# Kernel tuning notes

Measured on AMD Instinct MI355X. Metric: run time of the kernel, lower is better.

## Reference

```python
import jax, jax.numpy as jnp
import numpy as np

D = 1024      # input_dim == memory_dim
HID = 1024    # hid_dim
NEG = 1e30


def setup_inputs() -> dict:
    key = jax.random.key(0)
    ks = jax.random.split(key, 9)
    N, LD, LM = 8, 2048, 512
    s = 1.0 / np.sqrt(D)
    return {
        "input": jax.random.normal(ks[0], (N, LD, D), jnp.float32),
        "memory": jax.random.normal(ks[1], (N, LM, D), jnp.float32),
        "mask": jnp.ones((N, LM), jnp.float32),
        # input_linear_1 / memory_linear_1: Linear(d, 1, bias=False)
        "in1_w": jax.random.normal(ks[2], (D,), jnp.float32) * s,
        "mem1_w": jax.random.normal(ks[3], (D,), jnp.float32) * s,
        # input_linear_2 / memory_linear_2: Linear(d, hid, bias=True), stored [d, hid]
        "in2_w": jax.random.normal(ks[4], (D, HID), jnp.float32) * s,
        "in2_b": jax.random.normal(ks[5], (HID,), jnp.float32) * s,
        "mem2_w": jax.random.normal(ks[6], (D, HID), jnp.float32) * s,
        "mem2_b": jax.random.normal(ks[7], (HID,), jnp.float32) * s,
    }


def reference(input, memory, mask, in1_w, mem1_w, in2_w, in2_b, mem2_w, mem2_b):
    # dropout=0.0 / eval mode -> identity
    dot_scale = jnp.asarray(np.sqrt(D), input.dtype)
    input_dot = jnp.einsum("nld,d->nl", input, in1_w)[:, :, None]      # [N,Ld,1]
    memory_dot = jnp.einsum("nmd,d->nm", memory, mem1_w)[:, None, :]   # [N,1,Lm]
    cross_dot = jnp.einsum("nld,nmd->nlm", input, memory) / dot_scale  # [N,Ld,Lm]
    att = input_dot + memory_dot + cross_dot
    att = att - NEG * (1.0 - mask[:, None, :])

    inp2 = jnp.einsum("nld,dh->nlh", input, in2_w) + in2_b    # [N,Ld,hid]
    mem2 = jnp.einsum("nmd,dh->nmh", memory, mem2_w) + mem2_b  # [N,Lm,hid]

    weight_one = jax.nn.softmax(att, axis=-1)                 # [N,Ld,Lm]
    output_one = jnp.einsum("nlm,nmh->nlh", weight_one, mem2)  # [N,Ld,hid]

    weight_two = jax.nn.softmax(jnp.max(att, axis=-1), axis=-1)  # [N,Ld]
    output_two = jnp.einsum("nl,nlh->nh", weight_two, inp2)[:, None, :]  # [N,1,hid]

    out = jnp.concatenate(
        [inp2, output_one, inp2 * output_one, output_two * output_one], axis=-1
    )  # [N,Ld,4*hid]
    return out, mem2
```

## Files before the change

### kernel.cpp

```cpp
#include <hip/hip_runtime.h>

typedef unsigned short u16;
typedef __attribute__((ext_vector_type(8))) short short8;
typedef __attribute__((ext_vector_type(4))) float f32x4;
typedef __attribute__((ext_vector_type(4))) unsigned short u16x4;

#define NSEQ 8
#define LD 2048
#define LM 512
#define DD 1024
#define HID 1024
#define M1 (NSEQ*LD)
#define M2 (NSEQ*LM)

#define GLOAD_LDS16(gp, lp) __builtin_amdgcn_global_load_lds( \
    (const __attribute__((address_space(1))) unsigned int*)(gp), \
    (__attribute__((address_space(3))) unsigned int*)(lp), 16, 0, 0)

__device__ __forceinline__ u16 f2bf(float f) {
    union { float f; unsigned int i; } v; v.f = f;
    unsigned int r = v.i + 0x7fffu + ((v.i >> 16) & 1u);
    return (u16)(r >> 16);
}
__device__ __forceinline__ float bf2f(u16 u) {
    union { unsigned int i; float f; } v; v.i = ((unsigned int)u) << 16; return v.f;
}

__global__ __launch_bounds__(256) void prep_rows2(
    const float* __restrict__ input, const float* __restrict__ memory,
    const float* __restrict__ in1_w, const float* __restrict__ mem1_w,
    const float* __restrict__ mask,
    u16* __restrict__ input_bf16, u16* __restrict__ memory_bf16,
    float* __restrict__ idot, float* __restrict__ mdotm) {
    const int row = blockIdx.x, t = threadIdx.x;
    const float* src; const float* w; u16* dst;
    if (row < M1) { src = input + (size_t)row * DD; w = in1_w;
                    dst = input_bf16 + (size_t)row * DD; }
    else { const int rm = row - M1; src = memory + (size_t)rm * DD; w = mem1_w;
           dst = memory_bf16 + (size_t)rm * DD; }
    f32x4 v = *(const f32x4*)(src + t * 4);
    f32x4 wv = *(const f32x4*)(w + t * 4);
    u16x4 o;
    #pragma unroll
    for (int i = 0; i < 4; i++) o[i] = f2bf(v[i]);
    *(u16x4*)(dst + t * 4) = o;
    float s = v[0]*wv[0] + v[1]*wv[1] + v[2]*wv[2] + v[3]*wv[3];
    #pragma unroll
    for (int off = 32; off; off >>= 1) s += __shfl_down(s, off);
    __shared__ float red[4];
    if ((t & 63) == 0) red[t >> 6] = s;
    __syncthreads();
    if (t == 0) {
        const float d = red[0] + red[1] + red[2] + red[3];
        if (row < M1) idot[row] = d;
        else { const int rm = row - M1;
               mdotm[rm] = d - 1e30f * (1.0f - mask[rm]); }
    }
}

__global__ void wtrans(const float* __restrict__ s0, const float* __restrict__ s1,
                       u16* __restrict__ d0, u16* __restrict__ d1) {
    __shared__ float tile[32][33];
    const float* src = blockIdx.z ? s1 : s0;
    u16* dst = blockIdx.z ? d1 : d0;
    const int c0 = blockIdx.x * 32, r0 = blockIdx.y * 32;
    const int tx = threadIdx.x, ty = threadIdx.y;
    #pragma unroll
    for (int yy = ty; yy < 32; yy += 8)
        tile[yy][tx] = src[(size_t)(r0 + yy) * DD + c0 + tx];
    __syncthreads();
    #pragma unroll
    for (int yy = ty; yy < 32; yy += 8)
        dst[(size_t)(c0 + yy) * DD + r0 + tx] = f2bf(tile[tx][yy]);
}

__global__ void transpose_f32_to_bf16(const float* __restrict__ src,
                                      u16* __restrict__ dst,
                                      int R, int C, size_t sn, size_t dn) {
    __shared__ float tile[32][33];
    src += (size_t)blockIdx.z * sn;
    dst += (size_t)blockIdx.z * dn;
    const int c0 = blockIdx.x * 32, r0 = blockIdx.y * 32;
    const int tx = threadIdx.x, ty = threadIdx.y;
    #pragma unroll
    for (int yy = ty; yy < 32; yy += 8)
        tile[yy][tx] = src[(size_t)(r0 + yy) * C + c0 + tx];
    __syncthreads();
    #pragma unroll
    for (int yy = ty; yy < 32; yy += 8)
        dst[(size_t)(c0 + yy) * R + r0 + tx] = f2bf(tile[tx][yy]);
}

template <int NT>
__global__ __launch_bounds__(512, 1) void gemm256(
    const u16* __restrict__ A, const u16* __restrict__ B,
    int lda, int ldb,
    float* __restrict__ out0, int ldc, const float* __restrict__ bias) {
    constexpr int BUFE = (256 + 128) * 64;
    __shared__ __align__(16) u16 lds[3 * BUFE];
    const int t = threadIdx.x;
    const int lane = t & 63, wave = t >> 6;
    const int wm = wave >> 2, wn = wave & 3;
    const int lr = lane & 15, kg = lane >> 4;
    const int bid = blockIdx.y * 8 + blockIdx.x;
    const int swz = (bid & 7) * gridDim.y + (bid >> 3);
    const int m0 = (swz >> 3) * 256, n0 = (swz & 7) * 128;

    const int srow = lane >> 3;
    const u16* gA[4];
    const u16* gB[2];
    #pragma unroll
    for (int i = 0; i < 4; i++) {
        const int c = wave * 4 + i;
        const int colb = ((lane & 7) * 16) ^ ((((c << 2) + (lane >> 4)) & 7) << 4);
        gA[i] = A + (size_t)(m0 + c * 8 + srow) * lda + (colb >> 1);
    }
    #pragma unroll
    for (int i = 0; i < 2; i++) {
        const int c = wave * 2 + i;
        const int colb = ((lane & 7) * 16) ^ ((((c << 2) + (lane >> 4)) & 7) << 4);
        gB[i] = B + (size_t)(n0 + c * 8 + srow) * ldb + (colb >> 1);
    }
    int offA[8], offB[2];
    #pragma unroll
    for (int i = 0; i < 8; i++) {
        const int row = wm * 128 + i * 16 + lr;
        offA[i] = (row * 128 + kg * 16) ^ (((row >> 1) & 7) << 4);
    }
    #pragma unroll
    for (int j = 0; j < 2; j++) {
        const int row = wn * 32 + j * 16 + lr;
        offB[j] = (256 * 64 * 2 + row * 128 + kg * 16) ^ (((row >> 1) & 7) << 4);
    }

    f32x4 acc[8][2];
    #pragma unroll
    for (int i = 0; i < 8; i++)
        #pragma unroll
        for (int j = 0; j < 2; j++) acc[i][j] = (f32x4){0.f, 0.f, 0.f, 0.f};

    #define STAGE(tt, buf) do {                                             \
        u16* la_ = &lds[(buf) * BUFE];                                      \
        u16* lb_ = la_ + 256 * 64;                                          \
        const int ko_ = (tt) * 64;                                          \
        _Pragma("unroll")                                                   \
        for (int i_ = 0; i_ < 4; i_++)                                      \
            GLOAD_LDS16(gA[i_] + ko_, la_ + (wave * 4 + i_) * 512);         \
        _Pragma("unroll")                                                   \
        for (int i_ = 0; i_ < 2; i_++)                                      \
            GLOAD_LDS16(gB[i_] + ko_, lb_ + (wave * 2 + i_) * 512);         \
    } while (0)

    STAGE(0, 0);
    STAGE(1, 1);
    asm volatile("s_waitcnt vmcnt(6)" ::: "memory");
    __builtin_amdgcn_s_barrier();
    __builtin_amdgcn_sched_barrier(0);

    int cb = 0, sb = 2;
    for (int tt = 0; tt < NT; ++tt) {
        if (tt + 2 < NT) STAGE(tt + 2, sb);
        __builtin_amdgcn_sched_barrier(0);
        const char* bb = (const char*)&lds[cb * BUFE];
        short8 bfr[2][2];
        #pragma unroll
        for (int j = 0; j < 2; j++)
            #pragma unroll
            for (int kh = 0; kh < 2; kh++)
                bfr[j][kh] = *(const short8*)(bb + (offB[j] ^ (kh * 64)));
        #pragma unroll
        for (int p = 0; p < 4; p++) {
            short8 af[2][2];
            #pragma unroll
            for (int q = 0; q < 2; q++)
                #pragma unroll
                for (int kh = 0; kh < 2; kh++)
                    af[q][kh] = *(const short8*)(bb + (offA[2 * p + q] ^ (kh * 64)));
            __builtin_amdgcn_s_setprio(1);
            #pragma unroll
            for (int q = 0; q < 2; q++)
                #pragma unroll
                for (int j = 0; j < 2; j++)
                    #pragma unroll
                    for (int kh = 0; kh < 2; kh++)
                        acc[2 * p + q][j] = __builtin_amdgcn_mfma_f32_16x16x32_bf16(
                            af[q][kh], bfr[j][kh], acc[2 * p + q][j], 0, 0, 0);
            __builtin_amdgcn_s_setprio(0);
        }
        if (tt + 2 < NT)      asm volatile("s_waitcnt vmcnt(6)" ::: "memory");
        else if (tt + 1 < NT) asm volatile("s_waitcnt vmcnt(0)" ::: "memory");
        __builtin_amdgcn_s_barrier();
        __builtin_amdgcn_sched_barrier(0);
        cb = (cb == 2) ? 0 : cb + 1;
        sb = (sb == 2) ? 0 : sb + 1;
    }
    #undef STAGE

    #pragma unroll
    for (int i = 0; i < 8; i++) {
        #pragma unroll
        for (int j = 0; j < 2; j++) {
            const int col = n0 + wn * 32 + j * 16 + lr;
            #pragma unroll
            for (int r = 0; r < 4; r++) {
                const int row = m0 + wm * 128 + i * 16 + kg * 4 + r;
                out0[(size_t)row * ldc + col] = acc[i][j][r] + bias[col];
            }
        }
    }
}

__global__ __launch_bounds__(512, 2) void fused_gemm(
    const u16* __restrict__ A1, const u16* __restrict__ B1,
    const u16* __restrict__ A2, const u16* __restrict__ B2,
    float* __restrict__ out0,
    const float* __restrict__ bias, const float* __restrict__ ot) {
    constexpr int BUFE = (256 + 128) * 64;
    __shared__ __align__(16) u16 lds[3 * BUFE];
    const int t = threadIdx.x;
    const int lane = t & 63, wave = t >> 6;
    const int wm = wave >> 2, wn = wave & 3;
    const int lr = lane & 15, kg = lane >> 4;
    const int bid = blockIdx.y * 8 + blockIdx.x;
    const int swz = (bid & 7) * gridDim.y + (bid >> 3);
    const int m0 = (swz >> 3) * 256, n0 = (swz & 7) * 128;
    const int nb = m0 / LD;
    const u16* B2p = B2 + (size_t)nb * HID * LM;

    const int srow = lane >> 3;
    int colbA[4], colbB[2];
    const u16* gA[4];
    const u16* gB[2];
    #pragma unroll
    for (int i = 0; i < 4; i++) {
        const int c = wave * 4 + i;
        colbA[i] = ((lane & 7) * 16) ^ ((((c << 2) + (lane >> 4)) & 7) << 4);
        gA[i] = A1 + (size_t)(m0 + c * 8 + srow) * DD + (colbA[i] >> 1);
    }
    #pragma unroll
    for (int i = 0; i < 2; i++) {
        const int c = wave * 2 + i;
        colbB[i] = ((lane & 7) * 16) ^ ((((c << 2) + (lane >> 4)) & 7) << 4);
        gB[i] = B1 + (size_t)(n0 + c * 8 + srow) * DD + (colbB[i] >> 1);
    }
    int offA[8], offB[2];
    #pragma unroll
    for (int i = 0; i < 8; i++) {
        const int row = wm * 128 + i * 16 + lr;
        offA[i] = (row * 128 + kg * 16) ^ (((row >> 1) & 7) << 4);
    }
    #pragma unroll
    for (int j = 0; j < 2; j++) {
        const int row = wn * 32 + j * 16 + lr;
        offB[j] = (256 * 64 * 2 + row * 128 + kg * 16) ^ (((row >> 1) & 7) << 4);
    }

    #define STAGE(tt, buf) do {                                             \
        u16* la_ = &lds[(buf) * BUFE];                                      \
        u16* lb_ = la_ + 256 * 64;                                          \
        const int ko_ = (tt) * 64;                                          \
        _Pragma("unroll")                                                   \
        for (int i_ = 0; i_ < 4; i_++)                                      \
            GLOAD_LDS16(gA[i_] + ko_, la_ + (wave * 4 + i_) * 512);         \
        _Pragma("unroll")                                                   \
        for (int i_ = 0; i_ < 2; i_++)                                      \
            GLOAD_LDS16(gB[i_] + ko_, lb_ + (wave * 2 + i_) * 512);         \
    } while (0)

    #define KLOOP(NT, ACC)                                                  \
    do {                                                                    \
        STAGE(0, 0);                                                        \
        STAGE(1, 1);                                                        \
        asm volatile("s_waitcnt vmcnt(6)" ::: "memory");                    \
        __builtin_amdgcn_s_barrier();                                       \
        __builtin_amdgcn_sched_barrier(0);                                  \
        int cb = 0, sb = 2;                                                 \
        for (int tt = 0; tt < (NT); ++tt) {                                 \
            if (tt + 2 < (NT)) STAGE(tt + 2, sb);                           \
            __builtin_amdgcn_sched_barrier(0);                              \
            const char* bb = (const char*)&lds[cb * BUFE];                  \
            short8 bfr[2][2];                                               \
            _Pragma("unroll")                                               \
            for (int j = 0; j < 2; j++)                                     \
                _Pragma("unroll")                                           \
                for (int kh = 0; kh < 2; kh++)                              \
                    bfr[j][kh] = *(const short8*)(bb + (offB[j] ^ (kh * 64))); \
            _Pragma("unroll")                                               \
            for (int p = 0; p < 4; p++) {                                   \
                short8 af[2][2];                                            \
                _Pragma("unroll")                                           \
                for (int q = 0; q < 2; q++)                                 \
                    _Pragma("unroll")                                       \
                    for (int kh = 0; kh < 2; kh++)                          \
                        af[q][kh] = *(const short8*)(bb + (offA[2 * p + q] ^ (kh * 64))); \
                __builtin_amdgcn_s_setprio(1);                              \
                _Pragma("unroll")                                           \
                for (int q = 0; q < 2; q++)                                 \
                    _Pragma("unroll")                                       \
                    for (int j = 0; j < 2; j++)                             \
                        _Pragma("unroll")                                   \
                        for (int kh = 0; kh < 2; kh++)                      \
                            ACC[2 * p + q][j] = __builtin_amdgcn_mfma_f32_16x16x32_bf16( \
                                af[q][kh], bfr[j][kh], ACC[2 * p + q][j], 0, 0, 0); \
                __builtin_amdgcn_s_setprio(0);                              \
            }                                                               \
            if (tt + 2 < (NT))      asm volatile("s_waitcnt vmcnt(6)" ::: "memory"); \
            else if (tt + 1 < (NT)) asm volatile("s_waitcnt vmcnt(0)" ::: "memory"); \
            __builtin_amdgcn_s_barrier();                                   \
            __builtin_amdgcn_sched_barrier(0);                              \
            cb = (cb == 2) ? 0 : cb + 1;                                    \
            sb = (sb == 2) ? 0 : sb + 1;                                    \
        }                                                                   \
    } while (0)

    f32x4 acc1[8][2], acc2[8][2];
    #pragma unroll
    for (int i = 0; i < 8; i++)
        #pragma unroll
        for (int j = 0; j < 2; j++) {
            acc1[i][j] = (f32x4){0.f, 0.f, 0.f, 0.f};
            acc2[i][j] = (f32x4){0.f, 0.f, 0.f, 0.f};
        }

    KLOOP(16, acc1);

    #pragma unroll
    for (int i = 0; i < 4; i++) {
        const int c = wave * 4 + i;
        gA[i] = A2 + (size_t)(m0 + c * 8 + srow) * LM + (colbA[i] >> 1);
    }
    #pragma unroll
    for (int i = 0; i < 2; i++) {
        const int c = wave * 2 + i;
        gB[i] = B2p + (size_t)(n0 + c * 8 + srow) * LM + (colbB[i] >> 1);
    }

    KLOOP(8, acc2);

    #undef KLOOP
    #undef STAGE

    #pragma unroll
    for (int i = 0; i < 8; i++) {
        #pragma unroll
        for (int j = 0; j < 2; j++) {
            const int col = n0 + wn * 32 + j * 16 + lr;
            const float b = bias[col];
            const float otv = ot[nb * HID + col];
            #pragma unroll
            for (int r = 0; r < 4; r++) {
                const int row = m0 + wm * 128 + i * 16 + kg * 4 + r;
                const size_t o = (size_t)row * 4096 + col;
                const float i2 = acc1[i][j][r] + b;
                const float o1 = acc2[i][j][r];
                out0[o] = i2;
                out0[o + 1024] = o1;
                out0[o + 2048] = i2 * o1;
                out0[o + 3072] = otv * o1;
            }
        }
    }
}

__global__ __launch_bounds__(512, 1) void att_softmax(
    const u16* __restrict__ A, const u16* __restrict__ B,
    const float* __restrict__ idot, const float* __restrict__ mdotm,
    u16* __restrict__ P, float* __restrict__ rowmax) {
    constexpr int ABUF = 64 * 64;
    constexpr int BBUF = 512 * 64;
    constexpr int BUFE = ABUF + BBUF;
    __shared__ __align__(16) u16 lds[2 * BUFE];
    const int t = threadIdx.x, lane = t & 63, wave = t >> 6;
    const int wm = wave >> 2, wn = wave & 3;
    const int lr = lane & 15, kg = lane >> 4;
    const int bid = blockIdx.x;
    const int swz = (bid & 7) * 32 + (bid >> 3);
    const int m0 = swz * 64;
    const int nb = m0 >> 11;
    const u16* Bp = B + (size_t)nb * LM * DD;

    const int srow = lane >> 3;
    const u16* gA;
    {
        const int c = wave;
        const int colb = ((lane & 7) * 16) ^ ((((c << 2) + (lane >> 4)) & 7) << 4);
        gA = A + (size_t)(m0 + c * 8 + srow) * DD + (colb >> 1);
    }
    const u16* gB[8];
    #pragma unroll
    for (int i = 0; i < 8; i++) {
        const int c = wave * 8 + i;
        const int colb = ((lane & 7) * 16) ^ ((((c << 2) + (lane >> 4)) & 7) << 4);
        gB[i] = Bp + (size_t)(c * 8 + srow) * DD + (colb >> 1);
    }
    int offA[2], offB[8];
    #pragma unroll
    for (int i = 0; i < 2; i++) {
        const int row = wm * 32 + i * 16 + lr;
        offA[i] = (row * 128 + kg * 16) ^ (((row >> 1) & 7) << 4);
    }
    #pragma unroll
    for (int j = 0; j < 8; j++) {
        const int row = wn * 128 + j * 16 + lr;
        offB[j] = (ABUF * 2 + row * 128 + kg * 16) ^ (((row >> 1) & 7) << 4);
    }

    f32x4 acc[2][8];
    #pragma unroll
    for (int i = 0; i < 2; i++)
        #pragma unroll
        for (int j = 0; j < 8; j++) acc[i][j] = (f32x4){0.f, 0.f, 0.f, 0.f};

    #define ASTAGE(tt, buf) do {                                            \
        u16* la_ = &lds[(buf) * BUFE];                                      \
        const int ko_ = (tt) * 64;                                          \
        GLOAD_LDS16(gA + ko_, la_ + wave * 512);                            \
        u16* lb_ = la_ + ABUF;                                              \
        _Pragma("unroll")                                                   \
        for (int i_ = 0; i_ < 8; i_++)                                      \
            GLOAD_LDS16(gB[i_] + ko_, lb_ + (wave * 8 + i_) * 512);         \
    } while (0)

    ASTAGE(0, 0);
    asm volatile("s_waitcnt vmcnt(0)" ::: "memory");
    __builtin_amdgcn_s_barrier();
    __builtin_amdgcn_sched_barrier(0);

    for (int tt = 0; tt < 16; ++tt) {
        if (tt + 1 < 16) ASTAGE(tt + 1, (tt + 1) & 1);
        __builtin_amdgcn_sched_barrier(0);
        const char* bb = (const char*)&lds[(tt & 1) * BUFE];
        short8 af[2][2];
        #pragma unroll
        for (int i = 0; i < 2; i++)
            #pragma unroll
            for (int kh = 0; kh < 2; kh++)
                af[i][kh] = *(const short8*)(bb + (offA[i] ^ (kh * 64)));
        #pragma unroll
        for (int j = 0; j < 8; j++) {
            short8 bf[2];
            #pragma unroll
            for (int kh = 0; kh < 2; kh++)
                bf[kh] = *(const short8*)(bb + (offB[j] ^ (kh * 64)));
            __builtin_amdgcn_s_setprio(1);
            #pragma unroll
            for (int i = 0; i < 2; i++)
                #pragma unroll
                for (int kh = 0; kh < 2; kh++)
                    acc[i][j] = __builtin_amdgcn_mfma_f32_16x16x32_bf16(
                        af[i][kh], bf[kh], acc[i][j], 0, 0, 0);
            __builtin_amdgcn_s_setprio(0);
        }
        if (tt + 1 < 16) asm volatile("s_waitcnt vmcnt(0)" ::: "memory");
        __builtin_amdgcn_s_barrier();
        __builtin_amdgcn_sched_barrier(0);
    }
    #undef ASTAGE

    float* redm = (float*)lds;
    float* reds = redm + 256;
    float mdv[8];
    #pragma unroll
    for (int j = 0; j < 8; j++)
        mdv[j] = mdotm[nb * LM + wn * 128 + j * 16 + lr];
    float idv[8];
    #pragma unroll
    for (int i = 0; i < 2; i++)
        #pragma unroll
        for (int r = 0; r < 4; r++)
            idv[i * 4 + r] = idot[m0 + wm * 32 + i * 16 + kg * 4 + r];
    float pm[8];
    #pragma unroll
    for (int i = 0; i < 2; i++)
        #pragma unroll
        for (int r = 0; r < 4; r++) {
            float mx = -3.0e38f;
            #pragma unroll
            for (int j = 0; j < 8; j++) {
                const float v = acc[i][j][r] * 0.03125f + idv[i * 4 + r] + mdv[j];
                acc[i][j][r] = v;
                mx = fmaxf(mx, v);
            }
            pm[i * 4 + r] = mx;
        }
    #pragma unroll
    for (int w = 1; w < 16; w <<= 1)
        #pragma unroll
        for (int q = 0; q < 8; q++) pm[q] = fmaxf(pm[q], __shfl_xor(pm[q], w));
    if (lr == 0) {
        #pragma unroll
        for (int i = 0; i < 2; i++)
            #pragma unroll
            for (int r = 0; r < 4; r++)
                redm[(wm * 32 + i * 16 + kg * 4 + r) * 4 + wn] = pm[i * 4 + r];
    }
    __syncthreads();
    float Mr[8], ps[8];
    #pragma unroll
    for (int i = 0; i < 2; i++)
        #pragma unroll
        for (int r = 0; r < 4; r++) {
            const int row = wm * 32 + i * 16 + kg * 4 + r;
            const float a = fmaxf(redm[row * 4 + 0], redm[row * 4 + 1]);
            const float b = fmaxf(redm[row * 4 + 2], redm[row * 4 + 3]);
            Mr[i * 4 + r] = fmaxf(a, b);
            float s = 0.f;
            #pragma unroll
            for (int j = 0; j < 8; j++) {
                const float e = __expf(acc[i][j][r] - Mr[i * 4 + r]);
                acc[i][j][r] = e;
                s += e;
            }
            ps[i * 4 + r] = s;
        }
    #pragma unroll
    for (int w = 1; w < 16; w <<= 1)
        #pragma unroll
        for (int q = 0; q < 8; q++) ps[q] += __shfl_xor(ps[q], w);
    if (lr == 0) {
        #pragma unroll
        for (int i = 0; i < 2; i++)
            #pragma unroll
            for (int r = 0; r < 4; r++)
                reds[(wm * 32 + i * 16 + kg * 4 + r) * 4 + wn] = ps[i * 4 + r];
    }
    __syncthreads();
    #pragma unroll
    for (int i = 0; i < 2; i++)
        #pragma unroll
        for (int r = 0; r < 4; r++) {
            const int row = wm * 32 + i * 16 + kg * 4 + r;
            const float inv = 1.0f / (reds[row * 4 + 0] + reds[row * 4 + 1] +
                                      reds[row * 4 + 2] + reds[row * 4 + 3]);
            if (wn == 0 && lr == 0) rowmax[m0 + row] = Mr[i * 4 + r];
            #pragma unroll
            for (int j = 0; j < 8; j++)
                P[(size_t)(m0 + row) * LM + wn * 128 + j * 16 + lr] =
                    f2bf(acc[i][j][r] * inv);
        }
}

__global__ __launch_bounds__(256) void xbar_partial(
    const float* __restrict__ rowmax, const u16* __restrict__ X,
    float* __restrict__ part) {
    const int lz = blockIdx.x, n = blockIdx.y, t = threadIdx.x;
    const float* rm = rowmax + (size_t)n * LD;
    float v[8];
    float m = -3.0e38f;
    #pragma unroll
    for (int i = 0; i < 8; i++) { v[i] = rm[t + i * 256]; m = fmaxf(m, v[i]); }
    #pragma unroll
    for (int off = 32; off; off >>= 1) m = fmaxf(m, __shfl_down(m, off));
    __shared__ float sm[4], ss[4];
    __shared__ float wl[256];
    if ((t & 63) == 0) sm[t >> 6] = m;
    __syncthreads();
    const float M = fmaxf(fmaxf(sm[0], sm[1]), fmaxf(sm[2], sm[3]));
    float s = 0.f;
    #pragma unroll
    for (int i = 0; i < 8; i++) s += __expf(v[i] - M);
    #pragma unroll
    for (int off = 32; off; off >>= 1) s += __shfl_down(s, off);
    if ((t & 63) == 0) ss[t >> 6] = s;
    __syncthreads();
    const float invS = 1.0f / (ss[0] + ss[1] + ss[2] + ss[3]);
    wl[t] = __expf(rm[lz * 256 + t] - M) * invS;
    __syncthreads();
    const u16* xp = X + ((size_t)n * LD + lz * 256) * DD + t * 4;
    f32x4 acc = {0.f, 0.f, 0.f, 0.f};
    #pragma unroll 4
    for (int l = 0; l < 256; l++) {
        u16x4 x = *(const u16x4*)(xp + (size_t)l * DD);
        const float w = wl[l];
        acc[0] += w * bf2f(x[0]); acc[1] += w * bf2f(x[1]);
        acc[2] += w * bf2f(x[2]); acc[3] += w * bf2f(x[3]);
    }
    *(f32x4*)&part[((size_t)n * 8 + lz) * HID + t * 4] = acc;
}

__global__ __launch_bounds__(256) void ot_final2(
    const float* __restrict__ part, const u16* __restrict__ Wt,
    const float* __restrict__ bias, float* __restrict__ ot) {
    const int hc = blockIdx.x, n = blockIdx.y, t = threadIdx.x;
    __shared__ float xb[HID];
    f32x4 s = {0.f, 0.f, 0.f, 0.f};
    #pragma unroll
    for (int i = 0; i < 8; i++) {
        f32x4 p = *(const f32x4*)&part[((size_t)n * 8 + i) * HID + t * 4];
        s[0] += p[0]; s[1] += p[1]; s[2] += p[2]; s[3] += p[3];
    }
    *(f32x4*)&xb[t * 4] = s;
    __syncthreads();
    const int h = hc * 128 + (t >> 1);
    const int d0 = (t & 1) * 512;
    float a = 0.f;
    #pragma unroll 4
    for (int d = 0; d < 512; d += 8) {
        short8 w8 = *(const short8*)&Wt[(size_t)h * DD + d0 + d];
        #pragma unroll
        for (int j = 0; j < 8; j++) a += bf2f((u16)w8[j]) * xb[d0 + d + j];
    }
    a += __shfl_xor(a, 1);
    if ((t & 1) == 0) ot[(size_t)n * HID + h] = a + bias[h];
}

extern "C" void kernel_launch(void* const* d_in, const int* in_sizes, int n_in,
                              void* d_out, int out_size, void* d_ws, size_t ws_size,
                              hipStream_t stream) {
    const float* input  = (const float*)d_in[0];
    const float* memory = (const float*)d_in[1];
    const float* mask   = (const float*)d_in[2];
    const float* in1_w  = (const float*)d_in[3];
    const float* mem1_w = (const float*)d_in[4];
    const float* in2_w  = (const float*)d_in[5];
    const float* in2_b  = (const float*)d_in[6];
    const float* mem2_w = (const float*)d_in[7];
    const float* mem2_b = (const float*)d_in[8];

    float* out = (float*)d_out;
    float* outTail = out + (size_t)M1 * 4096;

    char* ws = (char*)d_ws;
    size_t off = 0;
    auto alloc = [&](size_t bytes) -> void* {
        void* p = ws + off;
        off = (off + bytes + 255) & ~(size_t)255;
        return p;
    };
    u16* input_bf16  = (u16*)alloc((size_t)M1 * DD * 2);
    u16* memory_bf16 = (u16*)alloc((size_t)M2 * DD * 2);
    u16* in2_wt      = (u16*)alloc((size_t)HID * DD * 2);
    u16* mem2_wt     = (u16*)alloc((size_t)HID * DD * 2);
    u16* mem2t       = (u16*)alloc((size_t)NSEQ * HID * LM * 2);
    u16* P           = (u16*)alloc((size_t)M1 * LM * 2);
    float* idot      = (float*)alloc((size_t)M1 * 4);
    float* mdotm     = (float*)alloc((size_t)M2 * 4);
    float* rowmax    = (float*)alloc((size_t)M1 * 4);
    float* ot        = (float*)alloc((size_t)NSEQ * HID * 4);
    float* part      = (float*)alloc((size_t)NSEQ * 8 * HID * 4);

    prep_rows2<<<M1 + M2, 256, 0, stream>>>(input, memory, in1_w, mem1_w, mask,
                                            input_bf16, memory_bf16, idot, mdotm);
    wtrans<<<dim3(32, 32, 2), dim3(32, 8), 0, stream>>>(in2_w, mem2_w, in2_wt, mem2_wt);
    gemm256<16><<<dim3(8, M2 / 256), 512, 0, stream>>>(
        memory_bf16, mem2_wt, DD, DD, outTail, HID, mem2_b);
    transpose_f32_to_bf16<<<dim3(HID / 32, LM / 32, NSEQ), dim3(32, 8), 0, stream>>>(
        outTail, mem2t, LM, HID, (size_t)LM * HID, (size_t)HID * LM);
    att_softmax<<<M1 / 64, 512, 0, stream>>>(
        input_bf16, memory_bf16, idot, mdotm, P, rowmax);
    xbar_partial<<<dim3(8, NSEQ), 256, 0, stream>>>(rowmax, input_bf16, part);
    ot_final2<<<dim3(8, NSEQ), 256, 0, stream>>>(part, in2_wt, in2_b, ot);
    fused_gemm<<<dim3(8, M1 / 256), 512, 0, stream>>>(
        input_bf16, in2_wt, P, mem2t, out, in2_b, ot);
}
```

Baseline: 218.7 us.

## Shrink mem2 GEMM tile, triple-buffer att_softmax in halves, widen xbar split

Templates the mem2 projection GEMM on its A-tile height and launches it with 128-row tiles, doubling the block count so more CUs are busy on the small M2 problem. Restructures att_softmax to process the 512 memory columns in two 256-column passes with a three-stage LDS pipeline instead of double buffering. This cuts LDS per stage and overlaps loads better, at the cost of reloading the A tile twice. Splits xbar_partial across 32 chunks per sequence instead of 8 for more parallelism, which makes ot_final2 sum more partials.

Result: faster. 203.4 us (-7.0%).

```diff
diff --git a/kernel.cpp b/kernel.cpp
--- a/kernel.cpp
+++ b/kernel.cpp
@@ -91,12 +91,13 @@
         dst[(size_t)(c0 + yy) * R + r0 + tx] = f2bf(tile[tx][yy]);
 }
 
-template <int NT>
-__global__ __launch_bounds__(512, 1) void gemm256(
+template <int NT, int AI>
+__global__ __launch_bounds__(512, 1) void gemmT(
     const u16* __restrict__ A, const u16* __restrict__ B,
     int lda, int ldb,
     float* __restrict__ out0, int ldc, const float* __restrict__ bias) {
-    constexpr int BUFE = (256 + 128) * 64;
+    constexpr int BM = AI * 64;
+    constexpr int BUFE = (BM + 128) * 64;
     __shared__ __align__(16) u16 lds[3 * BUFE];
     const int t = threadIdx.x;
     const int lane = t & 63, wave = t >> 6;
@@ -104,14 +105,14 @@
     const int lr = lane & 15, kg = lane >> 4;
     const int bid = blockIdx.y * 8 + blockIdx.x;
     const int swz = (bid & 7) * gridDim.y + (bid >> 3);
-    const int m0 = (swz >> 3) * 256, n0 = (swz & 7) * 128;
+    const int m0 = (swz >> 3) * BM, n0 = (swz & 7) * 128;
 
     const int srow = lane >> 3;
-    const u16* gA[4];
+    const u16* gA[AI];
     const u16* gB[2];
     #pragma unroll
-    for (int i = 0; i < 4; i++) {
-        const int c = wave * 4 + i;
+    for (int i = 0; i < AI; i++) {
+        const int c = wave * AI + i;
         const int colb = ((lane & 7) * 16) ^ ((((c << 2) + (lane >> 4)) & 7) << 4);
         gA[i] = A + (size_t)(m0 + c * 8 + srow) * lda + (colb >> 1);
     }
@@ -121,39 +122,43 @@
         const int colb = ((lane & 7) * 16) ^ ((((c << 2) + (lane >> 4)) & 7) << 4);
         gB[i] = B + (size_t)(n0 + c * 8 + srow) * ldb + (colb >> 1);
     }
-    int offA[8], offB[2];
-    #pragma unroll
-    for (int i = 0; i < 8; i++) {
-        const int row = wm * 128 + i * 16 + lr;
+    int offA[2 * AI], offB[2];
+    #pragma unroll
+    for (int i = 0; i < 2 * AI; i++) {
+        const int row = wm * (BM / 2) + i * 16 + lr;
         offA[i] = (row * 128 + kg * 16) ^ (((row >> 1) & 7) << 4);
     }
     #pragma unroll
     for (int j = 0; j < 2; j++) {
         const int row = wn * 32 + j * 16 + lr;
-        offB[j] = (256 * 64 * 2 + row * 128 + kg * 16) ^ (((row >> 1) & 7) << 4);
-    }
-
-    f32x4 acc[8][2];
-    #pragma unroll
-    for (int i = 0; i < 8; i++)
+        offB[j] = (BM * 64 * 2 + row * 128 + kg * 16) ^ (((row >> 1) & 7) << 4);
+    }
+
+    f32x4 acc[2 * AI][2];
+    #pragma unroll
+    for (int i = 0; i < 2 * AI; i++)
         #pragma unroll
         for (int j = 0; j < 2; j++) acc[i][j] = (f32x4){0.f, 0.f, 0.f, 0.f};
 
     #define STAGE(tt, buf) do {                                             \
         u16* la_ = &lds[(buf) * BUFE];                                      \
-        u16* lb_ = la_ + 256 * 64;                                          \
+        u16* lb_ = la_ + BM * 64;                                           \
         const int ko_ = (tt) * 64;                                          \
         _Pragma("unroll")                                                   \
-        for (int i_ = 0; i_ < 4; i_++)                                      \
-            GLOAD_LDS16(gA[i_] + ko_, la_ + (wave * 4 + i_) * 512);         \
+        for (int i_ = 0; i_ < AI; i_++)                                     \
+            GLOAD_LDS16(gA[i_] + ko_, la_ + (wave * AI + i_) * 512);        \
         _Pragma("unroll")                                                   \
         for (int i_ = 0; i_ < 2; i_++)                                      \
             GLOAD_LDS16(gB[i_] + ko_, lb_ + (wave * 2 + i_) * 512);         \
     } while (0)
+    #define WAITN() do {                                                    \
+        if constexpr (AI == 4) asm volatile("s_waitcnt vmcnt(6)" ::: "memory"); \
+        else                   asm volatile("s_waitcnt vmcnt(4)" ::: "memory"); \
+    } while (0)
 
     STAGE(0, 0);
     STAGE(1, 1);
-    asm volatile("s_waitcnt vmcnt(6)" ::: "memory");
+    WAITN();
     __builtin_amdgcn_s_barrier();
     __builtin_amdgcn_sched_barrier(0);
 
@@ -169,7 +174,7 @@
             for (int kh = 0; kh < 2; kh++)
                 bfr[j][kh] = *(const short8*)(bb + (offB[j] ^ (kh * 64)));
         #pragma unroll
-        for (int p = 0; p < 4; p++) {
+        for (int p = 0; p < AI; p++) {
             short8 af[2][2];
             #pragma unroll
             for (int q = 0; q < 2; q++)
@@ -187,7 +192,7 @@
                             af[q][kh], bfr[j][kh], acc[2 * p + q][j], 0, 0, 0);
             __builtin_amdgcn_s_setprio(0);
         }
-        if (tt + 2 < NT)      asm volatile("s_waitcnt vmcnt(6)" ::: "memory");
+        if (tt + 2 < NT)      WAITN();
         else if (tt + 1 < NT) asm volatile("s_waitcnt vmcnt(0)" ::: "memory");
         __builtin_amdgcn_s_barrier();
         __builtin_amdgcn_sched_barrier(0);
@@ -195,15 +200,16 @@
         sb = (sb == 2) ? 0 : sb + 1;
     }
     #undef STAGE
-
-    #pragma unroll
-    for (int i = 0; i < 8; i++) {
+    #undef WAITN
+
+    #pragma unroll
+    for (int i = 0; i < 2 * AI; i++) {
         #pragma unroll
         for (int j = 0; j < 2; j++) {
             const int col = n0 + wn * 32 + j * 16 + lr;
             #pragma unroll
             for (int r = 0; r < 4; r++) {
-                const int row = m0 + wm * 128 + i * 16 + kg * 4 + r;
+                const int row = m0 + wm * (BM / 2) + i * 16 + kg * 4 + r;
                 out0[(size_t)row * ldc + col] = acc[i][j][r] + bias[col];
             }
         }
@@ -367,9 +373,9 @@
     const float* __restrict__ idot, const float* __restrict__ mdotm,
     u16* __restrict__ P, float* __restrict__ rowmax) {
     constexpr int ABUF = 64 * 64;
-    constexpr int BBUF = 512 * 64;
+    constexpr int BBUF = 256 * 64;
     constexpr int BUFE = ABUF + BBUF;
-    __shared__ __align__(16) u16 lds[2 * BUFE];
+    __shared__ __align__(16) u16 lds[3 * BUFE];
     const int t = threadIdx.x, lane = t & 63, wave = t >> 6;
     const int wm = wave >> 2, wn = wave & 3;
     const int lr = lane & 15, kg = lane >> 4;
@@ -382,26 +388,25 @@
     const int srow = lane >> 3;
     const u16* gA;
     {
-        const int c = wave;
-        const int colb = ((lane & 7) * 16) ^ ((((c << 2) + (lane >> 4)) & 7) << 4);
-        gA = A + (size_t)(m0 + c * 8 + srow) * DD + (colb >> 1);
-    }
-    const u16* gB[8];
-    #pragma unroll
-    for (int i = 0; i < 8; i++) {
-        const int c = wave * 8 + i;
+        const int colb = ((lane & 7) * 16) ^ ((((wave << 2) + (lane >> 4)) & 7) << 4);
+        gA = A + (size_t)(m0 + wave * 8 + srow) * DD + (colb >> 1);
+    }
+    const u16* gB[4];
+    #pragma unroll
+    for (int i = 0; i < 4; i++) {
+        const int c = wave * 4 + i;
         const int colb = ((lane & 7) * 16) ^ ((((c << 2) + (lane >> 4)) & 7) << 4);
         gB[i] = Bp + (size_t)(c * 8 + srow) * DD + (colb >> 1);
     }
-    int offA[2], offB[8];
+    int offA[2], offB[4];
     #pragma unroll
     for (int i = 0; i < 2; i++) {
         const int row = wm * 32 + i * 16 + lr;
         offA[i] = (row * 128 + kg * 16) ^ (((row >> 1) & 7) << 4);
     }
     #pragma unroll
-    for (int j = 0; j < 8; j++) {
-        const int row = wn * 128 + j * 16 + lr;
+    for (int j = 0; j < 4; j++) {
+        const int row = wn * 64 + j * 16 + lr;
         offB[j] = (ABUF * 2 + row * 128 + kg * 16) ^ (((row >> 1) & 7) << 4);
     }
 
@@ -411,49 +416,56 @@
         #pragma unroll
         for (int j = 0; j < 8; j++) acc[i][j] = (f32x4){0.f, 0.f, 0.f, 0.f};
 
-    #define ASTAGE(tt, buf) do {                                            \
+    #define ASTAGE(tt, buf, pofs) do {                                      \
         u16* la_ = &lds[(buf) * BUFE];                                      \
+        u16* lb_ = la_ + ABUF;                                              \
         const int ko_ = (tt) * 64;                                          \
         GLOAD_LDS16(gA + ko_, la_ + wave * 512);                            \
-        u16* lb_ = la_ + ABUF;                                              \
         _Pragma("unroll")                                                   \
-        for (int i_ = 0; i_ < 8; i_++)                                      \
-            GLOAD_LDS16(gB[i_] + ko_, lb_ + (wave * 8 + i_) * 512);         \
+        for (int i_ = 0; i_ < 4; i_++)                                      \
+            GLOAD_LDS16(gB[i_] + (pofs) + ko_, lb_ + (wave * 4 + i_) * 512); \
     } while (0)
 
-    ASTAGE(0, 0);
-    asm volatile("s_waitcnt vmcnt(0)" ::: "memory");
-    __builtin_amdgcn_s_barrier();
-    __builtin_amdgcn_sched_barrier(0);
-
-    for (int tt = 0; tt < 16; ++tt) {
-        if (tt + 1 < 16) ASTAGE(tt + 1, (tt + 1) & 1);
+    for (int c = 0; c < 2; c++) {
+        const size_t pofs = (size_t)c * 256 * DD;
+        ASTAGE(0, 0, pofs);
+        ASTAGE(1, 1, pofs);
+        asm volatile("s_waitcnt vmcnt(5)" ::: "memory");
+        __builtin_amdgcn_s_barrier();
         __builtin_amdgcn_sched_barrier(0);
-        const char* bb = (const char*)&lds[(tt & 1) * BUFE];
-        short8 af[2][2];
-        #pragma unroll
-        for (int i = 0; i < 2; i++)
-            #pragma unroll
-            for (int kh = 0; kh < 2; kh++)
-                af[i][kh] = *(const short8*)(bb + (offA[i] ^ (kh * 64)));
-        #pragma unroll
-        for (int j = 0; j < 8; j++) {
-            short8 bf[2];
-            #pragma unroll
-            for (int kh = 0; kh < 2; kh++)
-                bf[kh] = *(const short8*)(bb + (offB[j] ^ (kh * 64)));
-            __builtin_amdgcn_s_setprio(1);
+        int cb = 0, sb = 2;
+        for (int tt = 0; tt < 16; ++tt) {
+            if (tt + 2 < 16) ASTAGE(tt + 2, sb, pofs);
+            __builtin_amdgcn_sched_barrier(0);
+            const char* bb = (const char*)&lds[cb * BUFE];
+            short8 af[2][2];
             #pragma unroll
             for (int i = 0; i < 2; i++)
                 #pragma unroll
                 for (int kh = 0; kh < 2; kh++)
-                    acc[i][j] = __builtin_amdgcn_mfma_f32_16x16x32_bf16(
-                        af[i][kh], bf[kh], acc[i][j], 0, 0, 0);
-            __builtin_amdgcn_s_setprio(0);
-        }
-        if (tt + 1 < 16) asm volatile("s_waitcnt vmcnt(0)" ::: "memory");
-        __builtin_amdgcn_s_barrier();
-        __builtin_amdgcn_sched_barrier(0);
+                    af[i][kh] = *(const short8*)(bb + (offA[i] ^ (kh * 64)));
+            #pragma unroll
+            for (int j = 0; j < 4; j++) {
+                short8 bf[2];
+                #pragma unroll
+                for (int kh = 0; kh < 2; kh++)
+                    bf[kh] = *(const short8*)(bb + (offB[j] ^ (kh * 64)));
+                __builtin_amdgcn_s_setprio(1);
+                #pragma unroll
+                for (int i = 0; i < 2; i++)
+                    #pragma unroll
+                    for (int kh = 0; kh < 2; kh++)
+                        acc[i][c * 4 + j] = __builtin_amdgcn_mfma_f32_16x16x32_bf16(
+                            af[i][kh], bf[kh], acc[i][c * 4 + j], 0, 0, 0);
+                __builtin_amdgcn_s_setprio(0);
+            }
+            if (tt + 2 < 16)      asm volatile("s_waitcnt vmcnt(5)" ::: "memory");
+            else if (tt + 1 < 16) asm volatile("s_waitcnt vmcnt(0)" ::: "memory");
+            __builtin_amdgcn_s_barrier();
+            __builtin_amdgcn_sched_barrier(0);
+            cb = (cb == 2) ? 0 : cb + 1;
+            sb = (sb == 2) ? 0 : sb + 1;
+        }
     }
     #undef ASTAGE
 
@@ -461,8 +473,8 @@
     float* reds = redm + 256;
     float mdv[8];
     #pragma unroll
-    for (int j = 0; j < 8; j++)
-        mdv[j] = mdotm[nb * LM + wn * 128 + j * 16 + lr];
+    for (int cj = 0; cj < 8; cj++)
+        mdv[cj] = mdotm[nb * LM + (cj >> 2) * 256 + wn * 64 + (cj & 3) * 16 + lr];
     float idv[8];
     #pragma unroll
     for (int i = 0; i < 2; i++)
@@ -476,9 +488,9 @@
         for (int r = 0; r < 4; r++) {
             float mx = -3.0e38f;
             #pragma unroll
-            for (int j = 0; j < 8; j++) {
-                const float v = acc[i][j][r] * 0.03125f + idv[i * 4 + r] + mdv[j];
-                acc[i][j][r] = v;
+            for (int cj = 0; cj < 8; cj++) {
+                const float v = acc[i][cj][r] * 0.03125f + idv[i * 4 + r] + mdv[cj];
+                acc[i][cj][r] = v;
                 mx = fmaxf(mx, v);
             }
             pm[i * 4 + r] = mx;
@@ -506,9 +518,9 @@
             Mr[i * 4 + r] = fmaxf(a, b);
             float s = 0.f;
             #pragma unroll
-            for (int j = 0; j < 8; j++) {
-                const float e = __expf(acc[i][j][r] - Mr[i * 4 + r]);
-                acc[i][j][r] = e;
+            for (int cj = 0; cj < 8; cj++) {
+                const float e = __expf(acc[i][cj][r] - Mr[i * 4 + r]);
+                acc[i][cj][r] = e;
                 s += e;
             }
             ps[i * 4 + r] = s;
@@ -534,9 +546,10 @@
                                       reds[row * 4 + 2] + reds[row * 4 + 3]);
             if (wn == 0 && lr == 0) rowmax[m0 + row] = Mr[i * 4 + r];
             #pragma unroll
-            for (int j = 0; j < 8; j++)
-                P[(size_t)(m0 + row) * LM + wn * 128 + j * 16 + lr] =
-                    f2bf(acc[i][j][r] * inv);
+            for (int cj = 0; cj < 8; cj++)
+                P[(size_t)(m0 + row) * LM +
+                  (cj >> 2) * 256 + wn * 64 + (cj & 3) * 16 + lr] =
+                    f2bf(acc[i][cj][r] * inv);
         }
 }
 
@@ -552,7 +565,7 @@
     #pragma unroll
     for (int off = 32; off; off >>= 1) m = fmaxf(m, __shfl_down(m, off));
     __shared__ float sm[4], ss[4];
-    __shared__ float wl[256];
+    __shared__ float wl[64];
     if ((t & 63) == 0) sm[t >> 6] = m;
     __syncthreads();
     const float M = fmaxf(fmaxf(sm[0], sm[1]), fmaxf(sm[2], sm[3]));
@@ -564,18 +577,18 @@
     if ((t & 63) == 0) ss[t >> 6] = s;
     __syncthreads();
     const float invS = 1.0f / (ss[0] + ss[1] + ss[2] + ss[3]);
-    wl[t] = __expf(rm[lz * 256 + t] - M) * invS;
-    __syncthreads();
-    const u16* xp = X + ((size_t)n * LD + lz * 256) * DD + t * 4;
+    if (t < 64) wl[t] = __expf(rm[lz * 64 + t] - M) * invS;
+    __syncthreads();
+    const u16* xp = X + ((size_t)n * LD + lz * 64) * DD + t * 4;
     f32x4 acc = {0.f, 0.f, 0.f, 0.f};
     #pragma unroll 4
-    for (int l = 0; l < 256; l++) {
+    for (int l = 0; l < 64; l++) {
         u16x4 x = *(const u16x4*)(xp + (size_t)l * DD);
         const float w = wl[l];
         acc[0] += w * bf2f(x[0]); acc[1] += w * bf2f(x[1]);
         acc[2] += w * bf2f(x[2]); acc[3] += w * bf2f(x[3]);
     }
-    *(f32x4*)&part[((size_t)n * 8 + lz) * HID + t * 4] = acc;
+    *(f32x4*)&part[((size_t)n * 32 + lz) * HID + t * 4] = acc;
 }
 
 __global__ __launch_bounds__(256) void ot_final2(
@@ -585,8 +598,8 @@
     __shared__ float xb[HID];
     f32x4 s = {0.f, 0.f, 0.f, 0.f};
     #pragma unroll
-    for (int i = 0; i < 8; i++) {
-        f32x4 p = *(const f32x4*)&part[((size_t)n * 8 + i) * HID + t * 4];
+    for (int i = 0; i < 32; i++) {
+        f32x4 p = *(const f32x4*)&part[((size_t)n * 32 + i) * HID + t * 4];
         s[0] += p[0]; s[1] += p[1]; s[2] += p[2]; s[3] += p[3];
     }
     *(f32x4*)&xb[t * 4] = s;
@@ -637,18 +650,18 @@
     float* mdotm     = (float*)alloc((size_t)M2 * 4);
     float* rowmax    = (float*)alloc((size_t)M1 * 4);
     float* ot        = (float*)alloc((size_t)NSEQ * HID * 4);
-    float* part      = (float*)alloc((size_t)NSEQ * 8 * HID * 4);
+    float* part      = (float*)alloc((size_t)NSEQ * 32 * HID * 4);
 
     prep_rows2<<<M1 + M2, 256, 0, stream>>>(input, memory, in1_w, mem1_w, mask,
                                             input_bf16, memory_bf16, idot, mdotm);
     wtrans<<<dim3(32, 32, 2), dim3(32, 8), 0, stream>>>(in2_w, mem2_w, in2_wt, mem2_wt);
-    gemm256<16><<<dim3(8, M2 / 256), 512, 0, stream>>>(
+    gemmT<16, 2><<<dim3(8, M2 / 128), 512, 0, stream>>>(
         memory_bf16, mem2_wt, DD, DD, outTail, HID, mem2_b);
     transpose_f32_to_bf16<<<dim3(HID / 32, LM / 32, NSEQ), dim3(32, 8), 0, stream>>>(
         outTail, mem2t, LM, HID, (size_t)LM * HID, (size_t)HID * LM);
     att_softmax<<<M1 / 64, 512, 0, stream>>>(
         input_bf16, memory_bf16, idot, mdotm, P, rowmax);
-    xbar_partial<<<dim3(8, NSEQ), 256, 0, stream>>>(rowmax, input_bf16, part);
+    xbar_partial<<<dim3(32, NSEQ), 256, 0, stream>>>(rowmax, input_bf16, part);
     ot_final2<<<dim3(8, NSEQ), 256, 0, stream>>>(part, in2_wt, in2_b, ot);
     fused_gemm<<<dim3(8, M1 / 256), 512, 0, stream>>>(
         input_bf16, in2_wt, P, mem2t, out, in2_b, ot);
```
